# Optimization experiments

Hardware: AMD Instinct MI355X
Metric: run time of the kernel (lower is better)

## Reference

```python
import jax, jax.numpy as jnp
import numpy as np

A0, A1, A2 = 1.0, 1.0, 0.5  # Taylor coefficients of exp around 0 (p=2)

B, H, N, D = 2, 16, 4096, 32


def setup_inputs() -> dict:
    key = jax.random.key(0)
    kq, kk, kv = jax.random.split(key, 3)
    q = jax.random.normal(kq, (B, H, N, D), dtype=jnp.float32)
    k = jax.random.normal(kk, (B, H, N, D), dtype=jnp.float32)
    v = jax.random.normal(kv, (B, H, N, D), dtype=jnp.float32)
    return {"q": q, "k": k, "v": v}


def reference(q, k, v):
    # fastmax_function with p=2, mask=False, normalize=False, dropout=0 -> temperature=1
    b, h, n, d = q.shape
    # quadratic feature maps: flatten of outer products, [b,h,n,d*d]
    q2 = (q[..., :, None] * q[..., None, :]).reshape(b, h, n, d * d)
    k2 = (k[..., :, None] * k[..., None, :]).reshape(b, h, n, d * d)
    # numerator: a0*sum(v) + a1*q(k^T v) + a2*q2(k2^T v)
    second_term = A1 * jnp.einsum('bhnd,bhne->bhde', k, v)           # [b,h,d,d]
    third_term = A2 * jnp.einsum('bhnf,bhne->bhfe', k2, v)           # [b,h,d^2,d]
    ans = (jnp.einsum('bhnd,bhde->bhne', q, second_term)
           + jnp.einsum('bhnf,bhfe->bhne', q2, third_term)
           + A0 * jnp.sum(v, axis=-2, keepdims=True))                 # [b,h,n,d]
    # denominator: a0*n + a1*q.sum(k) + a2*q2.sum(k2)
    div = (A0 * n
           + A1 * jnp.einsum('bhnd,bhd->bhn', q, jnp.sum(k, axis=-2))
           + A2 * jnp.einsum('bhnf,bhf->bhn', q2, jnp.sum(k2, axis=-2)))  # [b,h,n]
    return ans / div[..., None]
```

## Files before the change

### kernel.cpp

```cpp
#include <hip/hip_runtime.h>

#define NTOK 4096
#define NBH  32
#define NF   576
#define NE   33
#define NKT  18
#define GTF_BH (NKT * 3 * 64 * 8)

typedef _Float16 half_t;
typedef _Float16 half8 __attribute__((ext_vector_type(8)));
typedef _Float16 half4v __attribute__((ext_vector_type(4)));
typedef float f32x4 __attribute__((ext_vector_type(4)));
typedef unsigned int u32;

#define MFMA16(A,B,C) __builtin_amdgcn_mfma_f32_16x16x32_f16((A),(B),(C),0,0,0)

#define ASYNC_CP16(dst_lds, src_glb) \
    __builtin_amdgcn_global_load_lds( \
        (const __attribute__((address_space(1))) u32*)(const void*)(src_glb), \
        (__attribute__((address_space(3))) u32*)(void*)(dst_lds), 16, 0, 0)

static __device__ __forceinline__ half8 splat8(half_t x) {
    return (half8){x, x, x, x, x, x, x, x};
}

__global__ __launch_bounds__(256)
void t_kernel(const float* __restrict__ kin, const float* __restrict__ vin,
              half_t* __restrict__ kTg, half_t* __restrict__ vTg)
{
    const int nb = blockIdx.x;
    const int bh = blockIdx.y;
    const int t  = threadIdx.x;
    __shared__ __align__(16) half_t tile[32 * 272];
    const size_t inbase = ((size_t)bh * NTOK + nb * 256) * 32;

    for (int pass = 0; pass < 2; ++pass) {
        const float* src = pass ? vin : kin;
        half_t* dstg     = pass ? vTg : kTg;
        if (pass) __syncthreads();
        const float4* s4 = (const float4*)(src + inbase);
        #pragma unroll
        for (int r = 0; r < 8; ++r) {
            int f4 = t + 256 * r;
            int n = f4 >> 3, d4 = f4 & 7;
            float4 vv = s4[f4];
            int nn = n ^ ((d4 & 7) << 3);
            int d0 = d4 * 4;
            tile[(d0 + 0) * 272 + nn] = (half_t)vv.x;
            tile[(d0 + 1) * 272 + nn] = (half_t)vv.y;
            tile[(d0 + 2) * 272 + nn] = (half_t)vv.z;
            tile[(d0 + 3) * 272 + nn] = (half_t)vv.w;
        }
        __syncthreads();
        #pragma unroll
        for (int cc = 0; cc < 4; ++cc) {
            int lin = t + 256 * cc;
            int d = lin >> 5, ch = lin & 31;
            int sw = (d >> 2) & 7;
            half8 val = *(const half8*)&tile[d * 272 + ((ch ^ sw) << 3)];
            *(half8*)&dstg[((size_t)bh * 32 + d) * NTOK + nb * 256 + ch * 8] = val;
        }
    }
}

__global__ __launch_bounds__(256, 2)
void a_kernel(const half_t* __restrict__ kTg, const half_t* __restrict__ vTg,
              half_t* __restrict__ P, int Kc)
{
    const int x  = blockIdx.x;
    const int bh = x & (NBH - 1);
    const int kc = x >> 5;
    const int t = threadIdx.x;
    const int w = t >> 6, lane = t & 63, l16 = lane & 15, quad = lane >> 4;
    const int pw = w * 144;

    __shared__ __align__(16) half_t kT0[2 * 4096];
    __shared__ __align__(16) half_t vT0[2 * 4096];

    const half8 h05 = splat8((half_t)0.5f);
    f32x4 acc[9][3];
    #pragma unroll
    for (int m = 0; m < 9; ++m)
        #pragma unroll
        for (int e = 0; e < 3; ++e)
            acc[m][e] = (f32x4){0.f, 0.f, 0.f, 0.f};

    int rotoff[9], rotsalt[9];
    #pragma unroll
    for (int mt = 0; mt < 9; ++mt) {
        const int pm = pw + mt * 16;
        int ro = 0, rs = 0;
        if (pm >= 32 && pm < 512) {
            const int s  = 1 + ((pm - 32) >> 5);
            const int i0 = (pm - 32) & 31;
            const int r  = (i0 + l16 + s) & 31;
            ro = r * 128;
            rs = r & 15;
        }
        rotoff[mt] = ro;
        rotsalt[mt] = rs;
    }

    const size_t gbase = (size_t)bh * 32 * NTOK;
    const int nPer = NTOK / Kc;
    const int nStages = nPer >> 7;

    const int c0 = t,        r0 = c0 >> 4, p0s = (c0 & 15) ^ (r0 & 15);
    const int c1 = 256 + t,  r1 = c1 >> 4, p1s = (c1 & 15) ^ (r1 & 15);

    auto issue = [&](int buf, int nbase) {
        const half_t* gk0 = kTg + gbase + (size_t)r0 * NTOK + nbase + p0s * 8;
        const half_t* gk1 = kTg + gbase + (size_t)r1 * NTOK + nbase + p1s * 8;
        const half_t* gv0 = vTg + gbase + (size_t)r0 * NTOK + nbase + p0s * 8;
        const half_t* gv1 = vTg + gbase + (size_t)r1 * NTOK + nbase + p1s * 8;
        half_t* kb = kT0 + buf * 4096;
        half_t* vb = vT0 + buf * 4096;
        ASYNC_CP16(kb + (size_t)w * 512,        gk0);
        ASYNC_CP16(kb + 2048 + (size_t)w * 512, gk1);
        ASYNC_CP16(vb + (size_t)w * 512,        gv0);
        ASYNC_CP16(vb + 2048 + (size_t)w * 512, gv1);
    };

    issue(0, kc * nPer);

    for (int st = 0; st < nStages; ++st) {
        const int cur = st & 1;
        __syncthreads();
        if (st + 1 < nStages) issue(cur ^ 1, kc * nPer + (st + 1) * 128);
        const half_t* kb = kT0 + cur * 4096;
        const half_t* vb = vT0 + cur * 4096;
        #pragma unroll
        for (int kk = 0; kk < 4; ++kk) {
            const int c = kk * 4 + quad;
            const int shL = ((c ^ l16) << 3);
            half8 kj0 = *(const half8*)&kb[l16 * 128 + shL];
            half8 kj1 = *(const half8*)&kb[(l16 + 16) * 128 + shL];
            half8 bf0 = *(const half8*)&vb[l16 * 128 + shL];
            half8 bf1 = *(const half8*)&vb[(l16 + 16) * 128 + shL];
            half_t onec = (l16 == 0) ? (half_t)1 : (half_t)0;
            half8 bf2 = splat8(onec);
            #pragma unroll
            for (int mt = 0; mt < 9; ++mt) {
                const int pm = pw + mt * 16;
                half8 af;
                if (pm < 32) {
                    af = pm ? kj1 : kj0;
                } else if (pm < 512) {
                    half8 rot = *(const half8*)&kb[rotoff[mt] + ((c ^ rotsalt[mt]) << 3)];
                    af = (((pm - 32) & 16) ? kj1 : kj0) * rot;
                } else if (pm == 512) {
                    af = kj0 * kj1;
                } else if (pm == 528) {
                    af = (kj0 * h05) * kj0;
                } else if (pm == 544) {
                    af = (kj1 * h05) * kj1;
                } else {
                    af = bf2;
                }
                acc[mt][0] = MFMA16(af, bf0, acc[mt][0]);
                acc[mt][1] = MFMA16(af, bf1, acc[mt][1]);
                acc[mt][2] = MFMA16(af, bf2, acc[mt][2]);
            }
        }
    }

    half_t* Pb = P + ((size_t)kc * NBH + bh) * NE * NF;
    #pragma unroll
    for (int mt = 0; mt < 9; ++mt) {
        int p0 = pw + mt * 16 + quad * 4;
        half4v h0 = {(half_t)acc[mt][0][0], (half_t)acc[mt][0][1],
                     (half_t)acc[mt][0][2], (half_t)acc[mt][0][3]};
        half4v h1 = {(half_t)acc[mt][1][0], (half_t)acc[mt][1][1],
                     (half_t)acc[mt][1][2], (half_t)acc[mt][1][3]};
        *(half4v*)&Pb[(size_t)l16 * NF + p0] = h0;
        *(half4v*)&Pb[(size_t)(l16 + 16) * NF + p0] = h1;
        if (l16 == 0) {
            half4v h2 = {(half_t)acc[mt][2][0], (half_t)acc[mt][2][1],
                         (half_t)acc[mt][2][2], (half_t)acc[mt][2][3]};
            *(half4v*)&Pb[(size_t)32 * NF + p0] = h2;
        }
    }
}

__global__ __launch_bounds__(256)
void ar_kernel(const half_t* __restrict__ P, half_t* __restrict__ GtF, int Kc)
{
    const int NP8 = NBH * NE * NF / 8;
    const int idx = blockIdx.x * 256 + threadIdx.x;
    if (idx >= NP8) return;
    float s[8] = {0.f, 0.f, 0.f, 0.f, 0.f, 0.f, 0.f, 0.f};
    for (int c = 0; c < Kc; ++c) {
        half8 h = *(const half8*)&P[(size_t)c * (NBH * NE * NF) + (size_t)idx * 8];
        #pragma unroll
        for (int j = 0; j < 8; ++j) s[j] += (float)h[j];
    }
    half8 o;
    #pragma unroll
    for (int j = 0; j < 8; ++j) o[j] = (half_t)s[j];
    int row = idx / 72;
    int p8 = idx - row * 72;
    int e = row % 33, bhh = row / 33;
    int kt = p8 >> 2, quad = p8 & 3;
    int rr = e >> 4, l16 = e & 15;
    size_t dst8 = (size_t)bhh * (GTF_BH / 8)
                + (size_t)(kt * 3 + rr) * 64 + quad * 16 + l16;
    *(half8*)&GtF[dst8 * 8] = o;
}

__global__ __launch_bounds__(256)
void b_kernel(const float* __restrict__ qin, const half_t* __restrict__ GtF,
              float* __restrict__ out)
{
    const int bh = blockIdx.x, mbq = blockIdx.y;
    const int t = threadIdx.x, w = t >> 6, lane = t & 63;
    const int l16 = lane & 15, quad = lane >> 4;
    __shared__ __align__(16) half_t qs2[256 * 56];
    __shared__ float denl[256];
    const size_t nbase = (size_t)bh * NTOK + mbq * 256;

    const float4* q4 = (const float4*)(qin + nbase * 32);
    #pragma unroll
    for (int r = 0; r < 8; ++r) {
        int f4 = t + 256 * r, n = f4 >> 3, d4 = f4 & 7;
        float4 vv = q4[f4];
        half4v h = {(half_t)vv.x, (half_t)vv.y, (half_t)vv.z, (half_t)vv.w};
        *(half4v*)&qs2[n * 56 + d4 * 4] = h;
        if (d4 < 4) *(half4v*)&qs2[n * 56 + 32 + d4 * 4] = h;
    }
    __syncthreads();

    const int rbase = w * 64;
    int tb[4];
    #pragma unroll
    for (int mt = 0; mt < 4; ++mt) tb[mt] = (rbase + mt * 16 + l16) * 56;

    half8 vq[4], hv[4], gv[4];
    #pragma unroll
    for (int mt = 0; mt < 4; ++mt) {
        const int qb = tb[mt] + quad * 8;
        vq[mt] = *(const half8*)&qs2[qb];
        hv[mt] = *(const half8*)&qs2[qb + 8];
        gv[mt] = *(const half8*)&qs2[qb + 16];
    }

    f32x4 acc[3][4];
    #pragma unroll
    for (int a = 0; a < 3; ++a)
        #pragma unroll
        for (int b = 0; b < 4; ++b)
            acc[a][b] = (f32x4){0.f, 0.f, 0.f, 0.f};

    const half_t* Gb = GtF + (size_t)bh * GTF_BH + (size_t)lane * 8;

#define LDF(kt, B) do { \
    _Pragma("unroll") \
    for (int rr = 0; rr < 3; ++rr) \
        (B)[rr] = *(const half8*)&Gb[(size_t)(((kt) * 3 + rr) * 64) * 8]; \
} while (0)

#define DO_MFMA(AF) do { \
    _Pragma("unroll") \
    for (int mt = 0; mt < 4; ++mt) { \
        acc[0][mt] = MFMA16((AF)[mt], B0[0], acc[0][mt]); \
        acc[1][mt] = MFMA16((AF)[mt], B0[1], acc[1][mt]); \
        acc[2][mt] = MFMA16((AF)[mt], B0[2], acc[2][mt]); \
    } \
} while (0)

#define RING() do { \
    _Pragma("unroll") \
    for (int rr = 0; rr < 3; ++rr) { B0[rr] = B1[rr]; B1[rr] = B2[rr]; B2[rr] = B3[rr]; } \
} while (0)

    half8 B0[3], B1[3], B2[3], B3[3];
    LDF(0, B0); LDF(1, B1); LDF(2, B2);

    {
        LDF(3, B3);
        DO_MFMA(vq);
        RING();
    }

#define QCHUNK(S) do { \
    if ((S) + 3 <= 17) LDF((S) + 3, B3); \
    half8 af[4]; \
    _Pragma("unroll") \
    for (int mt = 0; mt < 4; ++mt) { \
        half8 lo = ((S) < 8) ? vq[mt] : hv[mt]; \
        half8 hi = ((S) < 8) ? hv[mt] : gv[mt]; \
        half8 rot = __builtin_shufflevector(lo, hi, \
            ((S) & 7) + 0, ((S) & 7) + 1, ((S) & 7) + 2, ((S) & 7) + 3, \
            ((S) & 7) + 4, ((S) & 7) + 5, ((S) & 7) + 6, ((S) & 7) + 7); \
        af[mt] = vq[mt] * rot; \
    } \
    DO_MFMA(af); \
    RING(); \
} while (0)

    QCHUNK(1);  QCHUNK(2);  QCHUNK(3);  QCHUNK(4);  QCHUNK(5);
    QCHUNK(6);  QCHUNK(7);  QCHUNK(8);  QCHUNK(9);  QCHUNK(10);
    QCHUNK(11); QCHUNK(12); QCHUNK(13); QCHUNK(14); QCHUNK(15);

    {
        half8 af[4];
        #pragma unroll
        for (int mt = 0; mt < 4; ++mt) {
            const int off = tb[mt] + ((quad >= 2) ? (quad - 2) : quad) * 8;
            half8 Ld = *(const half8*)&qs2[off];
            af[mt] = (quad < 2) ? (vq[mt] * gv[mt]) : (Ld * Ld);
        }
        DO_MFMA(af);
        RING();
    }
    {
        const half8 zero = {};
        half8 c10 = {};
        c10[0] = (half_t)1;
        half8 af[4];
        #pragma unroll
        for (int mt = 0; mt < 4; ++mt) {
            half8 d = gv[mt] * gv[mt];
            af[mt] = (quad < 2) ? d : ((quad == 2) ? c10 : zero);
        }
        DO_MFMA(af);
    }
#undef QCHUNK
#undef RING
#undef DO_MFMA
#undef LDF

    if (l16 == 0) {
        #pragma unroll
        for (int mt = 0; mt < 4; ++mt)
            #pragma unroll
            for (int r = 0; r < 4; ++r)
                denl[rbase + mt * 16 + quad * 4 + r] = acc[2][mt][r];
    }
    __syncthreads();
    #pragma unroll
    for (int mt = 0; mt < 4; ++mt) {
        float inv[4];
        #pragma unroll
        for (int r = 0; r < 4; ++r)
            inv[r] = __builtin_amdgcn_rcpf(denl[rbase + mt * 16 + quad * 4 + r]);
        #pragma unroll
        for (int r = 0; r < 4; ++r) {
            size_t ro = (nbase + rbase + mt * 16 + quad * 4 + r) * 32;
            out[ro + l16] = acc[0][mt][r] * inv[r];
            out[ro + l16 + 16] = acc[1][mt][r] * inv[r];
        }
    }
}

extern "C" void kernel_launch(void* const* d_in, const int* in_sizes, int n_in,
                              void* d_out, int out_size, void* d_ws, size_t ws_size,
                              hipStream_t stream)
{
    const float* q = (const float*)d_in[0];
    const float* k = (const float*)d_in[1];
    const float* v = (const float*)d_in[2];
    float* out = (float*)d_out;

    const size_t planeBytes = (size_t)NBH * NE * NF * 2;
    const size_t ktBytes = (size_t)NBH * 32 * NTOK * 2;
    const size_t gtBytes = (size_t)NBH * GTF_BH * 2;
    int Kc = 16;
    while (Kc > 1 && ((size_t)Kc * planeBytes + 2 * ktBytes + gtBytes) > ws_size)
        Kc >>= 1;

    half_t* P = (half_t*)d_ws;
    half_t* kTg = (half_t*)((char*)d_ws + (size_t)Kc * planeBytes);
    half_t* vTg = kTg + (size_t)NBH * 32 * NTOK;
    half_t* GtF = vTg + (size_t)NBH * 32 * NTOK;

    t_kernel<<<dim3(16, NBH), 256, 0, stream>>>(k, v, kTg, vTg);
    a_kernel<<<dim3(Kc * NBH), 256, 0, stream>>>(kTg, vTg, P, Kc);
    const int NP8 = NBH * NE * NF / 8;
    ar_kernel<<<(NP8 + 255) / 256, 256, 0, stream>>>(P, GtF, Kc);
    b_kernel<<<dim3(NBH, 16), 256, 0, stream>>>(q, GtF, out);
}
```

Baseline: 126.6 us.

## Fuse k/v fp16 transpose into the K2^T V accumulation kernel

Removes the separate transpose kernel that wrote fp16 transposed k and v to global memory. The accumulation kernel now reads fp32 k and v directly into registers, converts them, and writes them transposed with a new swizzle into double-buffered LDS. The next stage's global loads are overlapped with the current stage's MFMAs. This drops one launch and a global round trip, but the LDS scatter is done with scalar half stores, which may cause bank conflicts. Kc is hardcoded to 16 and the workspace-size fallback is removed.

```diff
diff --git a/kernel.cpp b/kernel.cpp
--- a/kernel.cpp
+++ b/kernel.cpp
@@ -6,78 +6,38 @@
 #define NE   33
 #define NKT  18
 #define GTF_BH (NKT * 3 * 64 * 8)
+#define KC   16
+#define NSTG 2
+#define NVB  (KC * NBH)
+#define NP8  (NBH * NE * NF / 8)
 
 typedef _Float16 half_t;
 typedef _Float16 half8 __attribute__((ext_vector_type(8)));
 typedef _Float16 half4v __attribute__((ext_vector_type(4)));
 typedef float f32x4 __attribute__((ext_vector_type(4)));
-typedef unsigned int u32;
 
 #define MFMA16(A,B,C) __builtin_amdgcn_mfma_f32_16x16x32_f16((A),(B),(C),0,0,0)
-
-#define ASYNC_CP16(dst_lds, src_glb) \
-    __builtin_amdgcn_global_load_lds( \
-        (const __attribute__((address_space(1))) u32*)(const void*)(src_glb), \
-        (__attribute__((address_space(3))) u32*)(void*)(dst_lds), 16, 0, 0)
 
 static __device__ __forceinline__ half8 splat8(half_t x) {
     return (half8){x, x, x, x, x, x, x, x};
 }
 
-__global__ __launch_bounds__(256)
-void t_kernel(const float* __restrict__ kin, const float* __restrict__ vin,
-              half_t* __restrict__ kTg, half_t* __restrict__ vTg)
+static __device__ __forceinline__ int FS(int d) { return (d + (d >> 3)) & 15; }
+
+__global__ __launch_bounds__(256, 2)
+void ta_kernel(const float* __restrict__ kin, const float* __restrict__ vin,
+               half_t* __restrict__ P)
 {
-    const int nb = blockIdx.x;
-    const int bh = blockIdx.y;
-    const int t  = threadIdx.x;
-    __shared__ __align__(16) half_t tile[32 * 272];
-    const size_t inbase = ((size_t)bh * NTOK + nb * 256) * 32;
-
-    for (int pass = 0; pass < 2; ++pass) {
-        const float* src = pass ? vin : kin;
-        half_t* dstg     = pass ? vTg : kTg;
-        if (pass) __syncthreads();
-        const float4* s4 = (const float4*)(src + inbase);
-        #pragma unroll
-        for (int r = 0; r < 8; ++r) {
-            int f4 = t + 256 * r;
-            int n = f4 >> 3, d4 = f4 & 7;
-            float4 vv = s4[f4];
-            int nn = n ^ ((d4 & 7) << 3);
-            int d0 = d4 * 4;
-            tile[(d0 + 0) * 272 + nn] = (half_t)vv.x;
-            tile[(d0 + 1) * 272 + nn] = (half_t)vv.y;
-            tile[(d0 + 2) * 272 + nn] = (half_t)vv.z;
-            tile[(d0 + 3) * 272 + nn] = (half_t)vv.w;
-        }
-        __syncthreads();
-        #pragma unroll
-        for (int cc = 0; cc < 4; ++cc) {
-            int lin = t + 256 * cc;
-            int d = lin >> 5, ch = lin & 31;
-            int sw = (d >> 2) & 7;
-            half8 val = *(const half8*)&tile[d * 272 + ((ch ^ sw) << 3)];
-            *(half8*)&dstg[((size_t)bh * 32 + d) * NTOK + nb * 256 + ch * 8] = val;
-        }
-    }
-}
-
-__global__ __launch_bounds__(256, 2)
-void a_kernel(const half_t* __restrict__ kTg, const half_t* __restrict__ vTg,
-              half_t* __restrict__ P, int Kc)
-{
-    const int x  = blockIdx.x;
-    const int bh = x & (NBH - 1);
-    const int kc = x >> 5;
+    __shared__ __align__(16) half_t kb0[2 * 4096];
+    __shared__ __align__(16) half_t vb0[2 * 4096];
+
+    const int vb = blockIdx.x;
+    const int bh = vb & (NBH - 1), kc = vb >> 5;
     const int t = threadIdx.x;
     const int w = t >> 6, lane = t & 63, l16 = lane & 15, quad = lane >> 4;
     const int pw = w * 144;
-
-    __shared__ __align__(16) half_t kT0[2 * 4096];
-    __shared__ __align__(16) half_t vT0[2 * 4096];
-
     const half8 h05 = splat8((half_t)0.5f);
+
     f32x4 acc[9][3];
     #pragma unroll
     for (int m = 0; m < 9; ++m)
@@ -95,48 +55,55 @@
             const int i0 = (pm - 32) & 31;
             const int r  = (i0 + l16 + s) & 31;
             ro = r * 128;
-            rs = r & 15;
+            rs = FS(r);
         }
         rotoff[mt] = ro;
         rotsalt[mt] = rs;
     }
-
-    const size_t gbase = (size_t)bh * 32 * NTOK;
-    const int nPer = NTOK / Kc;
-    const int nStages = nPer >> 7;
-
-    const int c0 = t,        r0 = c0 >> 4, p0s = (c0 & 15) ^ (r0 & 15);
-    const int c1 = 256 + t,  r1 = c1 >> 4, p1s = (c1 & 15) ^ (r1 & 15);
-
-    auto issue = [&](int buf, int nbase) {
-        const half_t* gk0 = kTg + gbase + (size_t)r0 * NTOK + nbase + p0s * 8;
-        const half_t* gk1 = kTg + gbase + (size_t)r1 * NTOK + nbase + p1s * 8;
-        const half_t* gv0 = vTg + gbase + (size_t)r0 * NTOK + nbase + p0s * 8;
-        const half_t* gv1 = vTg + gbase + (size_t)r1 * NTOK + nbase + p1s * 8;
-        half_t* kb = kT0 + buf * 4096;
-        half_t* vb = vT0 + buf * 4096;
-        ASYNC_CP16(kb + (size_t)w * 512,        gk0);
-        ASYNC_CP16(kb + 2048 + (size_t)w * 512, gk1);
-        ASYNC_CP16(vb + (size_t)w * 512,        gv0);
-        ASYNC_CP16(vb + 2048 + (size_t)w * 512, gv1);
+    const int sh0 = FS(l16), sh1 = FS(l16 + 16);
+
+    const size_t fbase = ((size_t)bh * NTOK + kc * 256) * 32;
+    const float4* k4 = (const float4*)kin + fbase / 4;
+    const float4* v4 = (const float4*)vin + fbase / 4;
+
+    float kaf[16], vaf[16];
+    auto loadst = [&](int s) {
+        const int base = s * 1024;
+        #pragma unroll
+        for (int r = 0; r < 4; ++r) {
+            float4 kk = k4[base + t + 256 * r];
+            float4 vv = v4[base + t + 256 * r];
+            kaf[4*r+0] = kk.x; kaf[4*r+1] = kk.y; kaf[4*r+2] = kk.z; kaf[4*r+3] = kk.w;
+            vaf[4*r+0] = vv.x; vaf[4*r+1] = vv.y; vaf[4*r+2] = vv.z; vaf[4*r+3] = vv.w;
+        }
     };
-
-    issue(0, kc * nPer);
-
-    for (int st = 0; st < nStages; ++st) {
-        const int cur = st & 1;
-        __syncthreads();
-        if (st + 1 < nStages) issue(cur ^ 1, kc * nPer + (st + 1) * 128);
-        const half_t* kb = kT0 + cur * 4096;
-        const half_t* vb = vT0 + cur * 4096;
+    auto writest = [&](int buf) {
+        half_t* kb = kb0 + buf * 4096;
+        half_t* vb2 = vb0 + buf * 4096;
+        #pragma unroll
+        for (int r = 0; r < 4; ++r) {
+            const int fi = t + 256 * r;
+            const int n = fi >> 3, d4 = fi & 7;
+            const int c = n >> 3, j = n & 7;
+            #pragma unroll
+            for (int i = 0; i < 4; ++i) {
+                const int d = 4 * d4 + i;
+                const int a = d * 128 + ((c ^ FS(d)) << 3) + j;
+                kb[a] = (half_t)kaf[4*r+i];
+                vb2[a] = (half_t)vaf[4*r+i];
+            }
+        }
+    };
+    auto compute = [&](int buf) {
+        const half_t* kb = kb0 + buf * 4096;
+        const half_t* vbp = vb0 + buf * 4096;
         #pragma unroll
         for (int kk = 0; kk < 4; ++kk) {
             const int c = kk * 4 + quad;
-            const int shL = ((c ^ l16) << 3);
-            half8 kj0 = *(const half8*)&kb[l16 * 128 + shL];
-            half8 kj1 = *(const half8*)&kb[(l16 + 16) * 128 + shL];
-            half8 bf0 = *(const half8*)&vb[l16 * 128 + shL];
-            half8 bf1 = *(const half8*)&vb[(l16 + 16) * 128 + shL];
+            half8 kj0 = *(const half8*)&kb[l16 * 128 + ((c ^ sh0) << 3)];
+            half8 kj1 = *(const half8*)&kb[(l16 + 16) * 128 + ((c ^ sh1) << 3)];
+            half8 bf0 = *(const half8*)&vbp[l16 * 128 + ((c ^ sh0) << 3)];
+            half8 bf1 = *(const half8*)&vbp[(l16 + 16) * 128 + ((c ^ sh1) << 3)];
             half_t onec = (l16 == 0) ? (half_t)1 : (half_t)0;
             half8 bf2 = splat8(onec);
             #pragma unroll
@@ -162,6 +129,16 @@
                 acc[mt][2] = MFMA16(af, bf2, acc[mt][2]);
             }
         }
+    };
+
+    loadst(0);
+    writest(0);
+    __syncthreads();
+    for (int st = 0; st < NSTG; ++st) {
+        const int cur = st & 1;
+        if (st + 1 < NSTG) loadst(st + 1);
+        compute(cur);
+        if (st + 1 < NSTG) { writest(cur ^ 1); __syncthreads(); }
     }
 
     half_t* Pb = P + ((size_t)kc * NBH + bh) * NE * NF;
@@ -183,13 +160,12 @@
 }
 
 __global__ __launch_bounds__(256)
-void ar_kernel(const half_t* __restrict__ P, half_t* __restrict__ GtF, int Kc)
+void ar_kernel(const half_t* __restrict__ P, half_t* __restrict__ GtF)
 {
-    const int NP8 = NBH * NE * NF / 8;
     const int idx = blockIdx.x * 256 + threadIdx.x;
     if (idx >= NP8) return;
     float s[8] = {0.f, 0.f, 0.f, 0.f, 0.f, 0.f, 0.f, 0.f};
-    for (int c = 0; c < Kc; ++c) {
+    for (int c = 0; c < KC; ++c) {
         half8 h = *(const half8*)&P[(size_t)c * (NBH * NE * NF) + (size_t)idx * 8];
         #pragma unroll
         for (int j = 0; j < 8; ++j) s[j] += (float)h[j];
@@ -361,21 +337,11 @@
     const float* v = (const float*)d_in[2];
     float* out = (float*)d_out;
 
-    const size_t planeBytes = (size_t)NBH * NE * NF * 2;
-    const size_t ktBytes = (size_t)NBH * 32 * NTOK * 2;
-    const size_t gtBytes = (size_t)NBH * GTF_BH * 2;
-    int Kc = 16;
-    while (Kc > 1 && ((size_t)Kc * planeBytes + 2 * ktBytes + gtBytes) > ws_size)
-        Kc >>= 1;
-
+    const size_t planeHalves = (size_t)NBH * NE * NF;
     half_t* P = (half_t*)d_ws;
-    half_t* kTg = (half_t*)((char*)d_ws + (size_t)Kc * planeBytes);
-    half_t* vTg = kTg + (size_t)NBH * 32 * NTOK;
-    half_t* GtF = vTg + (size_t)NBH * 32 * NTOK;
-
-    t_kernel<<<dim3(16, NBH), 256, 0, stream>>>(k, v, kTg, vTg);
-    a_kernel<<<dim3(Kc * NBH), 256, 0, stream>>>(kTg, vTg, P, Kc);
-    const int NP8 = NBH * NE * NF / 8;
-    ar_kernel<<<(NP8 + 255) / 256, 256, 0, stream>>>(P, GtF, Kc);
+    half_t* GtF = P + (size_t)KC * planeHalves;
+
+    ta_kernel<<<dim3(NVB), 256, 0, stream>>>(k, v, P);
+    ar_kernel<<<dim3((NP8 + 255) / 256), 256, 0, stream>>>(P, GtF);
     b_kernel<<<dim3(NBH, 16), 256, 0, stream>>>(q, GtF, out);
 }
```

After: 123.1 us. 2.8% less time.
